# Kernel tuning notes

Measured on AMD Instinct MI355X. Metric: run time of the kernel, lower is better.

Reference implementation:

```python
import jax, jax.numpy as jnp
import numpy as np

EPS_COV = 0.01  # module eps added to covariance diagonal
G, N_MEM = 8, 64  # groups, channels per group


def _pade_coeffs(m=5):
    # Taylor coefficients of sqrt(1 - x): c_k = (-1)^k * binom(1/2, k)
    c = np.zeros(2 * m + 1)
    c[0] = 1.0
    b = 1.0
    for k in range(1, 2 * m + 1):
        b *= (0.5 - (k - 1)) / k
        c[k] = ((-1) ** k) * b
    # Pade [m/m]: q_0 = 1, solve sum_j q_j c_{k-j} = 0 for k = m+1..2m
    A = np.zeros((m, m))
    rhs = np.zeros(m)
    for i in range(m):
        k = m + 1 + i
        for j in range(m):
            A[i, j] = c[k - (j + 1)]
        rhs[i] = -c[k]
    q = np.concatenate([[1.0], np.linalg.solve(A, rhs)])
    p = np.array([sum(q[j] * c[k - j] for j in range(min(k, m) + 1)) for k in range(m + 1)])
    return p, q

_PADE_P, _PADE_Q = _pade_coeffs(5)


def matrix_pade_approximant(p, I):
    # evaluates the [5/5] Pade approximant of sqrt at p (normalized SPD matrix)
    pp = jnp.asarray(_PADE_P, dtype=p.dtype)
    pq = jnp.asarray(_PADE_Q, dtype=p.dtype)
    p_app = I - p
    p_sqrt = pp[0] * I
    q_sqrt = pq[0] * I
    p_hat = p_app
    for i in range(5):
        p_sqrt = p_sqrt + pp[i + 1] * p_hat
        q_sqrt = q_sqrt + pq[i + 1] * p_hat
        p_hat = p_hat @ p_app
    return jnp.linalg.solve(q_sqrt, p_sqrt)


def mpa_sqrt(M):
    # batched matrix square root via Pade approximant (MPA_Lya.forward)
    normM = jnp.linalg.norm(M, axis=(1, 2))[:, None, None]
    n = M.shape[1]
    I = jnp.broadcast_to(jnp.eye(n, dtype=M.dtype), M.shape)
    return matrix_pade_approximant(M / normM, I) * jnp.sqrt(normM)


def setup_inputs() -> dict:
    key = jax.random.key(0)
    k1, k2 = jax.random.split(key)
    x = jax.random.normal(k1, (32, 512, 64, 64), dtype=jnp.float32)
    weight = jax.random.uniform(k2, (G, N_MEM, 1), dtype=jnp.float32)
    bias = jnp.zeros((G, N_MEM, 1), dtype=jnp.float32)
    return {"x": x, "weight": weight, "bias": bias}


def reference(x, weight, bias):
    N, C, H, W = x.shape
    n_mem = C // G
    xg = jnp.transpose(x, (1, 0, 2, 3)).reshape(G, n_mem, -1)  # (G, n_mem, N*H*W)
    mu = jnp.mean(xg, axis=2, keepdims=True)
    xg = xg - mu
    I = jnp.eye(n_mem, dtype=x.dtype)[None]
    xxt = jnp.einsum('gim,gjm->gij', xg, xg) / (N * H * W) + I * EPS_COV
    subspace = jnp.linalg.inv(mpa_sqrt(xxt))  # ZCA whitening matrix per group
    xr = jnp.einsum('gij,gjm->gim', subspace, xg)
    xr = xr * weight + bias
    xr = xr.reshape(C, N, H, W)
    return jnp.transpose(xr, (1, 0, 2, 3))
```

## Files before the change

kernel.cpp:

```cpp
#include <hip/hip_runtime.h>

#define NBATCH 32
#define CHAN   512
#define HWSZ   4096
#define NG     8
#define NM     64
#define MTOT   (NBATCH * HWSZ)
#define EPSC   0.01f
#define P68    68

typedef _Float16 f16;
typedef _Float16 f16x8 __attribute__((ext_vector_type(8)));
typedef float    f32x4 __attribute__((ext_vector_type(4)));

#define MFMA16(a, b, c) __builtin_amdgcn_mfma_f32_16x16x32_f16(a, b, c, 0, 0, 0)

__global__ __launch_bounds__(256) void gram_k(const float* __restrict__ x,
                                              float* __restrict__ gpart,
                                              float* __restrict__ spart) {
    __shared__ __align__(16) f16 tile[64 * 128];
    __shared__ float red[2][4096];

    const int bid  = blockIdx.x;
    const int g    = bid >> 6;
    const int n    = (bid >> 1) & 31;
    const int half = bid & 1;
    const float* xb = x + ((size_t)(n * CHAN + g * NM)) * HWSZ + half * 2048;

    const int t = threadIdx.x;
    const int w = t >> 6;
    const int l = t & 63;

    f32x4 acc[4][4];
#pragma unroll
    for (int i = 0; i < 4; ++i)
#pragma unroll
        for (int j = 0; j < 4; ++j) acc[i][j] = (f32x4){0.f, 0.f, 0.f, 0.f};
    float fsum[4] = {0.f, 0.f, 0.f, 0.f};

    for (int tt = 0; tt < 16; ++tt) {
        const float* xt = xb + tt * 128;
#pragma unroll
        for (int i = 0; i < 4; ++i) {
            const int p    = t + 256 * i;
            const int ch   = p >> 4;
            const int off8 = (p & 15) * 8;
            const float4 v0 = *(const float4*)(xt + (size_t)ch * HWSZ + off8);
            const float4 v1 = *(const float4*)(xt + (size_t)ch * HWSZ + off8 + 4);
            fsum[i] += (v0.x + v0.y) + (v0.z + v0.w) + (v1.x + v1.y) + (v1.z + v1.w);
            f16x8 hv;
            hv[0] = (f16)v0.x; hv[1] = (f16)v0.y; hv[2] = (f16)v0.z; hv[3] = (f16)v0.w;
            hv[4] = (f16)v1.x; hv[5] = (f16)v1.y; hv[6] = (f16)v1.z; hv[7] = (f16)v1.w;
            *(f16x8*)&tile[ch * 128 + (off8 ^ ((ch & 7) << 3))] = hv;
        }
        __syncthreads();

        f16x8 frag[4];
#pragma unroll
        for (int rb = 0; rb < 4; ++rb) {
            const int ch = rb * 16 + (l & 15);
            const int k0 = w * 32 + (l >> 4) * 8;
            frag[rb] = *(const f16x8*)&tile[ch * 128 + (k0 ^ ((ch & 7) << 3))];
        }
#pragma unroll
        for (int i = 0; i < 4; ++i)
#pragma unroll
            for (int j = 0; j < 4; ++j)
                acc[i][j] = MFMA16(frag[i], frag[j], acc[i][j]);
        __syncthreads();
    }

#pragma unroll
    for (int i = 0; i < 4; ++i) {
        fsum[i] += __shfl_xor(fsum[i], 1);
        fsum[i] += __shfl_xor(fsum[i], 2);
        fsum[i] += __shfl_xor(fsum[i], 4);
        fsum[i] += __shfl_xor(fsum[i], 8);
    }
    if ((l & 15) == 0) {
        const int chb = t >> 4;
#pragma unroll
        for (int i = 0; i < 4; ++i)
            spart[(size_t)bid * 64 + chb + 16 * i] = fsum[i];
    }

    if (w >= 2) {
#pragma unroll
        for (int i = 0; i < 4; ++i)
#pragma unroll
            for (int j = 0; j < 4; ++j)
#pragma unroll
                for (int r = 0; r < 4; ++r) {
                    const int row = i * 16 + (l >> 4) * 4 + r;
                    const int col = j * 16 + (l & 15);
                    red[w - 2][row * 64 + col] = acc[i][j][r];
                }
    }
    __syncthreads();
    if (w < 2) {
#pragma unroll
        for (int i = 0; i < 4; ++i)
#pragma unroll
            for (int j = 0; j < 4; ++j)
#pragma unroll
                for (int r = 0; r < 4; ++r) {
                    const int row = i * 16 + (l >> 4) * 4 + r;
                    const int col = j * 16 + (l & 15);
                    red[w][row * 64 + col] += acc[i][j][r];
                }
    }
    __syncthreads();
#pragma unroll
    for (int k = 0; k < 16; ++k) {
        const int e = t + 256 * k;
        gpart[(size_t)bid * 4096 + e] = red[0][e] + red[1][e];
    }
}

__global__ __launch_bounds__(256) void solve_k(const float* __restrict__ gpart,
                                               const float* __restrict__ spart,
                                               const float* __restrict__ wgt,
                                               const float* __restrict__ bias,
                                               f16* __restrict__ Tf,
                                               float* __restrict__ offv) {
    __shared__ __align__(16) float A[64 * P68];
    __shared__ __align__(16) float B[64 * P68];
    __shared__ __align__(16) float Cc[64 * P68];
    __shared__ __align__(16) float Dd[64 * P68];
    __shared__ float mus[64];
    __shared__ float red[4];
    __shared__ float tr16[16];

    const int g = blockIdx.x, t = threadIdx.x;

    float covv[16], cov2[16];
#pragma unroll
    for (int k = 0; k < 16; ++k) { covv[k] = 0.f; cov2[k] = 0.f; }
    for (int p = 0; p < 64; p += 2) {
        const float* gp0 = gpart + ((size_t)(g * 64 + p)) * 4096;
        const float* gp1 = gp0 + 4096;
#pragma unroll
        for (int k = 0; k < 16; ++k) {
            covv[k] += gp0[t + 256 * k];
            cov2[k] += gp1[t + 256 * k];
        }
    }
#pragma unroll
    for (int k = 0; k < 16; ++k) covv[k] += cov2[k];

    if (t < 64) {
        float ss = 0.f;
#pragma unroll 8
        for (int p = 0; p < 64; ++p) ss += spart[(size_t)(g * 64 + p) * 64 + t];
        mus[t] = ss * (1.0f / MTOT);
    }
    __syncthreads();

    float loc = 0.f;
#pragma unroll
    for (int k = 0; k < 16; ++k) {
        const int e = t + 256 * k;
        const int i = e >> 6, j = e & 63;
        const float cv = covv[k] * (1.0f / MTOT) - mus[i] * mus[j] + (i == j ? EPSC : 0.f);
        covv[k] = cv;
        loc += cv * cv;
    }
#pragma unroll
    for (int o = 32; o > 0; o >>= 1) loc += __shfl_down(loc, o);
    if ((t & 63) == 0) red[t >> 6] = loc;
    __syncthreads();
    const float normM = sqrtf(red[0] + red[1] + red[2] + red[3]);
    const float ninv  = 1.0f / normM;

#pragma unroll
    for (int k = 0; k < 16; ++k) {
        const int e = t + 256 * k;
        const int i = e >> 6, j = e & 63;
        const float pa = (i == j ? 1.f : 0.f) - covv[k] * ninv;
        A[i * P68 + j] = pa;
        B[i * P68 + j] = pa;
    }
    __syncthreads();

    const int ty = t >> 4, tx = t & 15;
    const int i0 = ty * 4, j0 = tx * 4;

    const float PP[6] = {1.f, -2.75f, 2.75f, -1.203125f, 0.21484375f, -0.0107421875f};
    const float QQ[6] = {1.f, -2.25f, 1.75f, -0.546875f, 0.05859375f, -0.0009765625f};

    float pacc[4][4], qacc[4][4];
#pragma unroll
    for (int ai = 0; ai < 4; ++ai)
#pragma unroll
        for (int bi = 0; bi < 4; ++bi) {
            const int i = i0 + ai, j = j0 + bi;
            const float pa = A[i * P68 + j];
            const float id = (i == j) ? 1.f : 0.f;
            pacc[ai][bi] = PP[0] * id + PP[1] * pa;
            qacc[ai][bi] = QQ[0] * id + QQ[1] * pa;
        }

    float* src = B;
    float* dst = Cc;
    for (int s = 0; s < 4; ++s) {
        float mm[4][4];
#pragma unroll
        for (int ai = 0; ai < 4; ++ai)
#pragma unroll
            for (int bi = 0; bi < 4; ++bi) mm[ai][bi] = 0.f;
        for (int kk = 0; kk < 64; ++kk) {
            const float4 a4 = *(const float4*)&src[kk * P68 + i0];
            const float4 b4 = *(const float4*)&A[kk * P68 + j0];
            const float av[4] = {a4.x, a4.y, a4.z, a4.w};
            const float bv[4] = {b4.x, b4.y, b4.z, b4.w};
#pragma unroll
            for (int ai = 0; ai < 4; ++ai)
#pragma unroll
                for (int bi = 0; bi < 4; ++bi)
                    mm[ai][bi] = fmaf(av[ai], bv[bi], mm[ai][bi]);
        }
#pragma unroll
        for (int ai = 0; ai < 4; ++ai) {
            float4 w4;
            w4.x = mm[ai][0]; w4.y = mm[ai][1]; w4.z = mm[ai][2]; w4.w = mm[ai][3];
            *(float4*)&dst[(i0 + ai) * P68 + j0] = w4;
        }
#pragma unroll
        for (int ai = 0; ai < 4; ++ai)
#pragma unroll
            for (int bi = 0; bi < 4; ++bi) {
                pacc[ai][bi] = fmaf(PP[s + 2], mm[ai][bi], pacc[ai][bi]);
                qacc[ai][bi] = fmaf(QQ[s + 2], mm[ai][bi], qacc[ai][bi]);
            }
        __syncthreads();
        float* tmpp = src; src = dst; dst = tmpp;
    }

    if (ty == tx)
        tr16[tx] = pacc[0][0] + pacc[1][1] + pacc[2][2] + pacc[3][3];
    __syncthreads();
    float trsum = 0.f;
#pragma unroll
    for (int i = 0; i < 16; ++i) trsum += tr16[i];
    const float cP  = trsum * (1.0f / 64.0f);
    const float icP = 1.0f / cP;

#pragma unroll
    for (int ai = 0; ai < 4; ++ai) {
        float4 we, wq;
        const int i = i0 + ai;
        we.x = pacc[ai][0] * icP - (i == j0 + 0 ? 1.f : 0.f);
        we.y = pacc[ai][1] * icP - (i == j0 + 1 ? 1.f : 0.f);
        we.z = pacc[ai][2] * icP - (i == j0 + 2 ? 1.f : 0.f);
        we.w = pacc[ai][3] * icP - (i == j0 + 3 ? 1.f : 0.f);
        wq.x = qacc[ai][0]; wq.y = qacc[ai][1]; wq.z = qacc[ai][2]; wq.w = qacc[ai][3];
        *(float4*)&A[i * P68 + j0] = we;
        *(float4*)&B[i * P68 + j0] = wq;
    }
    __syncthreads();

    float* rsrc = B;
    float* rdst = Cc;
    for (int it = 0; it < 4; ++it) {
        float mm[4][4];
#pragma unroll
        for (int ai = 0; ai < 4; ++ai)
#pragma unroll
            for (int bi = 0; bi < 4; ++bi) mm[ai][bi] = 0.f;
        for (int kk = 0; kk < 64; ++kk) {
            const float4 a4 = *(const float4*)&A[kk * P68 + i0];
            const float4 b4 = *(const float4*)&rsrc[kk * P68 + j0];
            const float av[4] = {a4.x, a4.y, a4.z, a4.w};
            const float bv[4] = {b4.x, b4.y, b4.z, b4.w};
#pragma unroll
            for (int ai = 0; ai < 4; ++ai)
#pragma unroll
                for (int bi = 0; bi < 4; ++bi)
                    mm[ai][bi] = fmaf(av[ai], bv[bi], mm[ai][bi]);
        }
#pragma unroll
        for (int ai = 0; ai < 4; ++ai) {
            const float4 q4 = *(const float4*)&B[(i0 + ai) * P68 + j0];
            float4 w4;
            w4.x = q4.x - mm[ai][0]; w4.y = q4.y - mm[ai][1];
            w4.z = q4.z - mm[ai][2]; w4.w = q4.w - mm[ai][3];
            *(float4*)&rdst[(i0 + ai) * P68 + j0] = w4;
        }
        __syncthreads();
        if (it == 0) { rsrc = Cc; rdst = Dd; }
        else { float* tmpp = rsrc; rsrc = rdst; rdst = tmpp; }
    }
    float* X = rsrc;

    const float invs = icP / sqrtf(normM);
    if (t < 64) {
        float sm = 0.f;
        for (int j = 0; j < 64; ++j) sm += X[t * P68 + j] * mus[j];
        offv[g * NM + t] = bias[g * NM + t] - sm * invs * wgt[g * NM + t];
    }
#pragma unroll
    for (int k = 0; k < 16; ++k) {
        const int e = t + 256 * k;
        const int i = e >> 6, j = e & 63;
        Tf[(size_t)g * 4096 + e] = (f16)(X[i * P68 + j] * invs * wgt[g * NM + i]);
    }
}

__global__ __launch_bounds__(256) void apply_k(const float* __restrict__ x,
                                               const f16* __restrict__ Tf,
                                               const float* __restrict__ offv,
                                               float* __restrict__ out) {
    __shared__ __align__(16) f16 xs[128 * 64];
    __shared__ __align__(16) f16 Ts[4096];
    __shared__ float offs[64];

    const int bid  = 511 - (int)blockIdx.x;
    const int g    = bid >> 6;
    const int n    = (bid >> 1) & 31;
    const int half = bid & 1;
    const size_t base = ((size_t)(n * CHAN + g * NM)) * HWSZ + half * 2048;
    const float* xb = x + base;
    float* ob = out + base;

    const int t = threadIdx.x;
    const int w = t >> 6;
    const int l = t & 63;

#pragma unroll
    for (int i = 0; i < 2; ++i) {
        const int c   = t + 256 * i;
        const int oc  = c >> 3;
        const int icb = (c & 7) * 8;
        const f16x8 v = *(const f16x8*)&Tf[(size_t)g * 4096 + oc * 64 + icb];
        *(f16x8*)&Ts[oc * 64 + (icb ^ ((oc & 7) << 3))] = v;
    }
    if (t < 64) offs[t] = offv[g * NM + t];
    __syncthreads();

    f16x8 afrag[2];
#pragma unroll
    for (int c = 0; c < 2; ++c) {
        const int oc = w * 16 + (l & 15);
        const int k0 = c * 32 + (l >> 4) * 8;
        afrag[c] = *(const f16x8*)&Ts[oc * 64 + (k0 ^ ((oc & 7) << 3))];
    }
    float offr[4];
#pragma unroll
    for (int r = 0; r < 4; ++r) offr[r] = offs[w * 16 + (l >> 4) * 4 + r];

    for (int tt = 0; tt < 16; ++tt) {
        const float* xt = xb + tt * 128;
        __syncthreads();
#pragma unroll
        for (int i = 0; i < 4; ++i) {
            const int p    = t + 256 * i;
            const int ch   = p >> 4;
            const int off8 = (p & 15) * 8;
            const float4 v0 = *(const float4*)(xt + (size_t)ch * HWSZ + off8);
            const float4 v1 = *(const float4*)(xt + (size_t)ch * HWSZ + off8 + 4);
            f16 h[8];
            h[0] = (f16)v0.x; h[1] = (f16)v0.y; h[2] = (f16)v0.z; h[3] = (f16)v0.w;
            h[4] = (f16)v1.x; h[5] = (f16)v1.y; h[6] = (f16)v1.z; h[7] = (f16)v1.w;
#pragma unroll
            for (int j = 0; j < 8; ++j) {
                const int pos = off8 + j;
                xs[pos * 64 + (ch ^ (((pos ^ (pos >> 3)) & 7) << 3))] = h[j];
            }
        }
        __syncthreads();

#pragma unroll
        for (int pb = 0; pb < 8; ++pb) {
            f32x4 acc;
            acc[0] = offr[0]; acc[1] = offr[1]; acc[2] = offr[2]; acc[3] = offr[3];
            const int pos = pb * 16 + (l & 15);
            const int swz = ((pos ^ (pos >> 3)) & 7) << 3;
#pragma unroll
            for (int c = 0; c < 2; ++c) {
                const int k0 = c * 32 + (l >> 4) * 8;
                const f16x8 bfrag = *(const f16x8*)&xs[pos * 64 + (k0 ^ swz)];
                acc = MFMA16(afrag[c], bfrag, acc);
            }
            const int posg = tt * 128 + pb * 16 + (l & 15);
#pragma unroll
            for (int r = 0; r < 4; ++r) {
                const int oc = w * 16 + (l >> 4) * 4 + r;
                ob[(size_t)oc * HWSZ + posg] = acc[r];
            }
        }
    }
}

extern "C" void kernel_launch(void* const* d_in, const int* in_sizes, int n_in,
                              void* d_out, int out_size, void* d_ws, size_t ws_size,
                              hipStream_t stream) {
    const float* x    = (const float*)d_in[0];
    const float* wgt  = (const float*)d_in[1];
    const float* bias = (const float*)d_in[2];
    float* out = (float*)d_out;

    float* ws    = (float*)d_ws;
    float* gpart = ws;
    float* spart = ws + 2097152;
    float* offv  = ws + 2129920;
    f16*   Tf    = (f16*)(ws + 2130432);

    gram_k <<<512, 256, 0, stream>>>(x, gpart, spart);
    solve_k<<<8,   256, 0, stream>>>(gpart, spart, wgt, bias, Tf, offv);
    apply_k<<<512, 256, 0, stream>>>(x, Tf, offv, out);
}
```

Before: 232.2 us.

## Double-buffer gram tile loads and split apply kernel into more blocks

The gram kernel now uses two LDS tile buffers. It issues the global loads for the next 128-column chunk before running the MFMAs on the current one, overlapping memory latency with compute. The apply kernel is launched with 1024 blocks, each handling a quarter of a sample's spatial extent instead of a half, to raise parallelism across CUs. This costs more LDS and registers in gram_k, which may lower occupancy, and adds more per-block setup (Tf load) in apply_k.

```diff
diff --git a/kernel.cpp b/kernel.cpp
--- a/kernel.cpp
+++ b/kernel.cpp
@@ -18,7 +18,7 @@
 __global__ __launch_bounds__(256) void gram_k(const float* __restrict__ x,
                                               float* __restrict__ gpart,
                                               float* __restrict__ spart) {
-    __shared__ __align__(16) f16 tile[64 * 128];
+    __shared__ __align__(16) f16 tile[2][64 * 128];
     __shared__ float red[2][4096];
 
     const int bid  = blockIdx.x;
@@ -31,6 +31,9 @@
     const int w = t >> 6;
     const int l = t & 63;
 
+    const int chS   = t >> 4;
+    const int off8S = (t & 15) * 8;
+
     f32x4 acc[4][4];
 #pragma unroll
     for (int i = 0; i < 4; ++i)
@@ -38,35 +41,58 @@
         for (int j = 0; j < 4; ++j) acc[i][j] = (f32x4){0.f, 0.f, 0.f, 0.f};
     float fsum[4] = {0.f, 0.f, 0.f, 0.f};
 
+#pragma unroll
+    for (int i = 0; i < 4; ++i) {
+        const int ch = chS + 16 * i;
+        const float4 v0 = *(const float4*)(xb + (size_t)ch * HWSZ + off8S);
+        const float4 v1 = *(const float4*)(xb + (size_t)ch * HWSZ + off8S + 4);
+        fsum[i] += (v0.x + v0.y) + (v0.z + v0.w) + (v1.x + v1.y) + (v1.z + v1.w);
+        f16x8 hv;
+        hv[0] = (f16)v0.x; hv[1] = (f16)v0.y; hv[2] = (f16)v0.z; hv[3] = (f16)v0.w;
+        hv[4] = (f16)v1.x; hv[5] = (f16)v1.y; hv[6] = (f16)v1.z; hv[7] = (f16)v1.w;
+        *(f16x8*)&tile[0][ch * 128 + (off8S ^ ((ch & 7) << 3))] = hv;
+    }
+    __syncthreads();
+
     for (int tt = 0; tt < 16; ++tt) {
-        const float* xt = xb + tt * 128;
-#pragma unroll
-        for (int i = 0; i < 4; ++i) {
-            const int p    = t + 256 * i;
-            const int ch   = p >> 4;
-            const int off8 = (p & 15) * 8;
-            const float4 v0 = *(const float4*)(xt + (size_t)ch * HWSZ + off8);
-            const float4 v1 = *(const float4*)(xt + (size_t)ch * HWSZ + off8 + 4);
-            fsum[i] += (v0.x + v0.y) + (v0.z + v0.w) + (v1.x + v1.y) + (v1.z + v1.w);
-            f16x8 hv;
-            hv[0] = (f16)v0.x; hv[1] = (f16)v0.y; hv[2] = (f16)v0.z; hv[3] = (f16)v0.w;
-            hv[4] = (f16)v1.x; hv[5] = (f16)v1.y; hv[6] = (f16)v1.z; hv[7] = (f16)v1.w;
-            *(f16x8*)&tile[ch * 128 + (off8 ^ ((ch & 7) << 3))] = hv;
-        }
-        __syncthreads();
-
+        float4 va[4][2];
+        if (tt < 15) {
+            const float* xt = xb + (tt + 1) * 128;
+#pragma unroll
+            for (int i = 0; i < 4; ++i) {
+                const int ch = chS + 16 * i;
+                va[i][0] = *(const float4*)(xt + (size_t)ch * HWSZ + off8S);
+                va[i][1] = *(const float4*)(xt + (size_t)ch * HWSZ + off8S + 4);
+            }
+        }
+
+        const f16* tb = tile[tt & 1];
         f16x8 frag[4];
 #pragma unroll
         for (int rb = 0; rb < 4; ++rb) {
             const int ch = rb * 16 + (l & 15);
             const int k0 = w * 32 + (l >> 4) * 8;
-            frag[rb] = *(const f16x8*)&tile[ch * 128 + (k0 ^ ((ch & 7) << 3))];
+            frag[rb] = *(const f16x8*)&tb[ch * 128 + (k0 ^ ((ch & 7) << 3))];
         }
 #pragma unroll
         for (int i = 0; i < 4; ++i)
 #pragma unroll
             for (int j = 0; j < 4; ++j)
                 acc[i][j] = MFMA16(frag[i], frag[j], acc[i][j]);
+
+        if (tt < 15) {
+            f16* tn = tile[(tt + 1) & 1];
+#pragma unroll
+            for (int i = 0; i < 4; ++i) {
+                const int ch = chS + 16 * i;
+                const float4 v0 = va[i][0], v1 = va[i][1];
+                fsum[i] += (v0.x + v0.y) + (v0.z + v0.w) + (v1.x + v1.y) + (v1.z + v1.w);
+                f16x8 hv;
+                hv[0] = (f16)v0.x; hv[1] = (f16)v0.y; hv[2] = (f16)v0.z; hv[3] = (f16)v0.w;
+                hv[4] = (f16)v1.x; hv[5] = (f16)v1.y; hv[6] = (f16)v1.z; hv[7] = (f16)v1.w;
+                *(f16x8*)&tn[ch * 128 + (off8S ^ ((ch & 7) << 3))] = hv;
+            }
+        }
         __syncthreads();
     }
 
@@ -314,11 +340,12 @@
     __shared__ __align__(16) f16 Ts[4096];
     __shared__ float offs[64];
 
-    const int bid  = 511 - (int)blockIdx.x;
-    const int g    = bid >> 6;
-    const int n    = (bid >> 1) & 31;
-    const int half = bid & 1;
-    const size_t base = ((size_t)(n * CHAN + g * NM)) * HWSZ + half * 2048;
+    const int bid  = 1023 - (int)blockIdx.x;
+    const int g    = bid >> 7;
+    const int rest = bid & 127;
+    const int n    = rest >> 2;
+    const int q    = rest & 3;
+    const size_t base = ((size_t)(n * CHAN + g * NM)) * HWSZ + q * 1024;
     const float* xb = x + base;
     float* ob = out + base;
 
@@ -348,7 +375,7 @@
 #pragma unroll
     for (int r = 0; r < 4; ++r) offr[r] = offs[w * 16 + (l >> 4) * 4 + r];
 
-    for (int tt = 0; tt < 16; ++tt) {
+    for (int tt = 0; tt < 8; ++tt) {
         const float* xt = xb + tt * 128;
         __syncthreads();
 #pragma unroll
@@ -405,7 +432,7 @@
     float* offv  = ws + 2129920;
     f16*   Tf    = (f16*)(ws + 2130432);
 
-    gram_k <<<512, 256, 0, stream>>>(x, gpart, spart);
-    solve_k<<<8,   256, 0, stream>>>(gpart, spart, wgt, bias, Tf, offv);
-    apply_k<<<512, 256, 0, stream>>>(x, Tf, offv, out);
+    gram_k <<<512,  256, 0, stream>>>(x, gpart, spart);
+    solve_k<<<8,    256, 0, stream>>>(gpart, spart, wgt, bias, Tf, offv);
+    apply_k<<<1024, 256, 0, stream>>>(x, Tf, offv, out);
 }
```

New measurement: 253.7 us. +9.2%, slower.
